# Kernel tuning notes

Measured on AMD Instinct MI355X. Metric: run time of the kernel, lower is better.

## Reference

```python
import jax, jax.numpy as jnp
import numpy as np

B, L, D, H = 2, 2048, 2048, 16
DH = D // H  # 128 per-head dim
EPS = 1e-5


def setup_inputs() -> dict:
    key = jax.random.key(0)
    ks = jax.random.split(key, 6)
    s = 0.02  # xavier-ish init scale with gain 2**-2.5
    return {
        "hidden_states": jax.random.normal(ks[0], (B, L, D), jnp.float32),
        "Wq": jax.random.normal(ks[1], (D, D), jnp.float32) * s,
        "Wk": jax.random.normal(ks[2], (D, D), jnp.float32) * s,
        "Wv": jax.random.normal(ks[3], (D, D), jnp.float32) * s,
        "Wb": jax.random.normal(ks[4], (D, H), jnp.float32) * s,
        "o_norm_weight": jnp.ones((DH,), jnp.float32),
        "Wo": jax.random.normal(ks[5], (D, D), jnp.float32) * s,
    }


def _delta_rule(q, k, v, beta):
    """Recurrent delta-rule linear attention.
    q,k,v: [B,H,L,Dh]; beta: [B,H,L]. Math identical to fused_chunk_delta_rule.
    S_t = S_{t-1} + k_t (beta_t * (v_t - S_{t-1}^T k_t))^T ;  o_t = S_t^T q_t
    """
    def step(S, inp):
        qt, kt, vt, bt = inp  # [B,H,Dh],[B,H,Dh],[B,H,Dh],[B,H]
        v_pred = jnp.einsum('bhk,bhkv->bhv', kt, S)
        delta = (vt - v_pred) * bt[..., None]
        S = S + kt[..., None] * delta[:, :, None, :]
        ot = jnp.einsum('bhk,bhkv->bhv', qt, S)
        return S, ot

    xs = (q.transpose(2, 0, 1, 3), k.transpose(2, 0, 1, 3),
          v.transpose(2, 0, 1, 3), beta.transpose(2, 0, 1))
    S0 = jnp.zeros(q.shape[:2] + (q.shape[-1], v.shape[-1]), q.dtype)
    _, o = jax.lax.scan(step, S0, xs)  # o: [L,B,H,Dh]
    return o.transpose(1, 2, 0, 3)  # [B,H,L,Dh]


def reference(hidden_states, Wq, Wk, Wv, Wb, o_norm_weight, Wo):
    b, l, d = hidden_states.shape
    h = Wb.shape[1]
    dh = d // h

    q = hidden_states @ Wq
    k = hidden_states @ Wk
    v = jax.nn.silu(hidden_states @ Wv)

    def heads(x):
        return x.reshape(b, l, h, dh).transpose(0, 2, 1, 3)  # b h l d

    q, k, v = heads(q), heads(k), heads(v)

    # qk_norm = 'l2' (torch F.normalize with eps clamp)
    def l2n(x):
        n = jnp.sqrt(jnp.sum(x * x, axis=-1, keepdims=True))
        return x / jnp.maximum(n, 1e-12)

    q, k = l2n(q), l2n(k)
    q = q * (dh ** -0.5)  # fla delta-rule default scale

    beta = jax.nn.sigmoid(hidden_states @ Wb).transpose(0, 2, 1)  # b h l

    o = _delta_rule(q, k, v, beta)  # b h l dh
    o = o.transpose(0, 2, 1, 3)  # b l h dh

    # RMSNorm over head_v_dim
    o = o * jax.lax.rsqrt(jnp.mean(o * o, axis=-1, keepdims=True) + EPS)
    o = o * o_norm_weight

    return o.reshape(b, l, d) @ Wo
```

## Files before the change

kernel.cpp:

```cpp
#include <hip/hip_runtime.h>
#include <hip/hip_bf16.h>
#include <cstdint>

#define DEV static __device__ __forceinline__

typedef unsigned short u16;
typedef unsigned int u32;
typedef __attribute__((ext_vector_type(8))) short short8;
typedef __attribute__((ext_vector_type(4))) float f32x4;

constexpr int Bn = 2, Ln = 2048, Dn = 2048, Hn = 16;
constexpr int Mrows = Bn * Ln;
constexpr int CHK = 64, NCK = Ln / CHK;
constexpr int NCHUNKS = Bn * Hn * NCK;

DEV float b2f(u16 s) { union { float f; u32 u; } x; x.u = ((u32)s) << 16; return x.f; }
DEV u16 f2b(float f) {
  union { float f; u32 u; } x; x.f = f; u32 u = x.u;
  return (u16)((u + 0x7fffu + ((u >> 16) & 1u)) >> 16);
}

DEV void cp16(const void* g, void* l) {
  __builtin_amdgcn_global_load_lds(
      (const __attribute__((address_space(1))) u32*)(unsigned long long)(g),
      (__attribute__((address_space(3))) u32*)(unsigned long long)(l), 16, 0, 0);
}

DEV f32x4 mfma16(short8 a, short8 b, f32x4 c) {
  return __builtin_amdgcn_mfma_f32_16x16x32_bf16(a, b, c, 0, 0, 0);
}

DEV short8 scale8(short8 v, float sc) {
  short8 o;
#pragma unroll
  for (int e = 0; e < 8; e++) o[e] = (short)f2b(b2f((u16)v[e]) * sc);
  return o;
}

__global__ void k_cvt(const float* __restrict__ src, u16* __restrict__ dst, int n8) {
  int i = blockIdx.x * blockDim.x + threadIdx.x;
  if (i >= n8) return;
  const float4* s4 = (const float4*)(src + (size_t)i * 8);
  float4 a = s4[0], b = s4[1];
  u16 o[8] = {f2b(a.x), f2b(a.y), f2b(a.z), f2b(a.w), f2b(b.x), f2b(b.y), f2b(b.z), f2b(b.w)};
  *(short8*)(dst + (size_t)i * 8) = *(short8*)o;
}

struct Trans2Args { const float* src[4]; u16* dst[4]; };
__global__ __launch_bounds__(256) void k_trans2(Trans2Args t) {
  __shared__ u16 tile[64][72];
  const float* src = t.src[blockIdx.z];
  u16* dst = t.dst[blockIdx.z];
  int r0 = blockIdx.y * 64, c0 = blockIdx.x * 64;
  int tid = threadIdx.x;
  int lr = tid >> 2, lc = (tid & 3) * 16;
  const float* s = src + (size_t)(r0 + lr) * 2048 + c0 + lc;
#pragma unroll
  for (int i = 0; i < 4; i++) {
    float4 v = *(const float4*)(s + i * 4);
    tile[lr][lc + i * 4 + 0] = f2b(v.x);
    tile[lr][lc + i * 4 + 1] = f2b(v.y);
    tile[lr][lc + i * 4 + 2] = f2b(v.z);
    tile[lr][lc + i * 4 + 3] = f2b(v.w);
  }
  __syncthreads();
  int orr = tid >> 2, oc = (tid & 3) * 16;
  u16* d = dst + (size_t)(c0 + orr) * 2048 + r0 + oc;
  u16 buf[16];
#pragma unroll
  for (int e = 0; e < 16; e++) buf[e] = tile[oc + e][orr];
  *(short8*)(d) = *(short8*)buf;
  *(short8*)(d + 8) = *(short8*)(buf + 8);
}

struct TransArgs {
  const float* src[1]; u16* dst[1]; int rows[1]; int cols[1];
};
__global__ void k_trans(TransArgs t) {
  __shared__ u16 tile[32][33];
  const float* src = t.src[0]; u16* dst = t.dst[0];
  int rows = t.rows[0], cols = t.cols[0];
  int r0 = blockIdx.y * 32, c0 = blockIdx.x * 32;
  if (r0 >= rows || c0 >= cols) return;
  int tx = threadIdx.x, ty = threadIdx.y;
  for (int i = ty; i < 32; i += 8) {
    int r = r0 + i, c = c0 + tx;
    if (r < rows && c < cols) tile[i][tx] = f2b(src[(size_t)r * cols + c]);
  }
  __syncthreads();
  for (int i = ty; i < 32; i += 8) {
    int r = c0 + i, c = r0 + tx;
    if (r < cols && c < rows) dst[(size_t)r * rows + c] = tile[tx][i];
  }
}

__global__ __launch_bounds__(256) void k_beta(const u16* __restrict__ hs,
                                              const u16* __restrict__ WbT,
                                              float* __restrict__ beta_g) {
  __shared__ float part[256];
  int tid = threadIdx.x, wave = tid >> 6, lane = tid & 63, quad = lane >> 4, l15 = lane & 15;
  int tok0 = blockIdx.x * 16;
  const u16* arow = hs + (size_t)(tok0 + l15) * Dn + wave * 512;
  const u16* brow = WbT + (size_t)l15 * Dn + wave * 512;
  f32x4 acc = {0.f, 0.f, 0.f, 0.f};
#pragma unroll
  for (int k = 0; k < 512; k += 32) {
    short8 af = *(const short8*)&arow[k + quad * 8];
    short8 bf = *(const short8*)&brow[k + quad * 8];
    acc = mfma16(af, bf, acc);
  }
  part[tid] = 0.f;
  __syncthreads();
#pragma unroll
  for (int r = 0; r < 4; r++) atomicAdd(&part[l15 * 16 + quad * 4 + r], acc[r]);
  __syncthreads();
  int h = tid >> 4, tr = tid & 15;
  int b = tok0 >> 11;
  int l = (tok0 + tr) & 2047;
  beta_g[(size_t)(b * Hn + h) * Ln + l] = 1.f / (1.f + __expf(-part[h * 16 + tr]));
}

struct Gemm2Args { const u16* A; const u16* Bt; u16* C; int K; };

__global__ __launch_bounds__(512, 2) void k_gemm2(Gemm2Args g) {
  __shared__ u16 ldsbuf[61440];
  const char* LB = (const char*)ldsbuf;
  const int K = g.K, NT = K / 64;
  const size_t Kb = (size_t)K * 2;
  int tid = threadIdx.x, wave = tid >> 6, lane = tid & 63;
  int quad = lane >> 4, l15 = lane & 15;
  int wm = wave >> 2, wn = wave & 3;

  int bid = blockIdx.x;
  int wg = (bid & 7) * 32 + (bid >> 3);
  int by = wg >> 4, bx = wg & 15;
  int m0 = by * 256, n0f = bx * 384;

  int r0 = tid >> 2;
  int cby = (((tid & 3) ^ ((tid >> 3) & 3)) * 16);
  const char* gA = (const char*)g.A + (size_t)(m0 + r0) * Kb + cby;
  const char* gB = (const char*)g.Bt + (size_t)(n0f + r0) * Kb + cby;

  auto stageA = [&](int slot, int t, int kh) {
    const char* src = gA + (size_t)t * 128 + kh * 64;
    u16* dst = &ldsbuf[slot * 8192 + tid * 8];
    cp16(src, dst);
    cp16(src + (size_t)128 * Kb, dst + 4096);
  };
  auto stageB = [&](int slot, int t, int kh) {
    const char* src = gB + (size_t)t * 128 + kh * 64;
    u16* dst = &ldsbuf[24576 + slot * 12288 + tid * 8];
    cp16(src, dst);
    cp16(src + (size_t)128 * Kb, dst + 4096);
    cp16(src + (size_t)256 * Kb, dst + 8192);
  };

  f32x4 acc0[4][6], acc1[4][6];
#pragma unroll
  for (int i = 0; i < 4; i++)
#pragma unroll
    for (int j = 0; j < 6; j++) {
      acc0[i][j] = (f32x4){0.f, 0.f, 0.f, 0.f};
      acc1[i][j] = (f32x4){0.f, 0.f, 0.f, 0.f};
    }

  int rsw = (l15 >> 1) & 3;
  int rA = (wm * 128 + l15) * 64 + ((quad ^ rsw) * 16);
  int rB = (wn * 96 + l15) * 64 + ((quad ^ rsw) * 16);

  stageA(0, 0, 0);
  stageB(0, 0, 0);
  stageA(1, 0, 1);
  stageB(1, 0, 1);

  short8 bf[6];
  int u0 = 0;
  for (int t = 0; t < NT; ++t) {
    int u1 = u0 + 1; if (u1 == 3) u1 = 0;
    int u2 = u1 + 1; if (u2 == 3) u2 = 0;
    bool pf = (t + 1 < NT);
    const char* aK0 = LB + u0 * 16384;
    const char* aK1 = LB + u1 * 16384;
    const char* bK0 = LB + 49152 + u0 * 24576;
    const char* bK1 = LB + 49152 + u1 * 24576;

    asm volatile("s_waitcnt vmcnt(5)" ::: "memory");
    __builtin_amdgcn_s_barrier();
    __builtin_amdgcn_sched_barrier(0);
    if (pf) stageA(u2, t + 1, 0);
    {
      short8 av[4];
#pragma unroll
      for (int i = 0; i < 4; i++) av[i] = *(const short8*)(aK0 + rA + i * 1024);
#pragma unroll
      for (int j = 0; j < 6; j++) bf[j] = *(const short8*)(bK0 + rB + j * 1024);
      __builtin_amdgcn_s_setprio(1);
#pragma unroll
      for (int i = 0; i < 4; i++)
#pragma unroll
        for (int j = 0; j < 6; j++) acc0[i][j] = mfma16(av[i], bf[j], acc0[i][j]);
      __builtin_amdgcn_s_setprio(0);
    }

    asm volatile("s_waitcnt vmcnt(5)" ::: "memory");
    __builtin_amdgcn_s_barrier();
    __builtin_amdgcn_sched_barrier(0);
    if (pf) stageB(u2, t + 1, 0);
    {
      short8 av[4];
#pragma unroll
      for (int i = 0; i < 4; i++) av[i] = *(const short8*)(aK0 + rA + 4096 + i * 1024);
      __builtin_amdgcn_s_setprio(1);
#pragma unroll
      for (int i = 0; i < 4; i++)
#pragma unroll
        for (int j = 0; j < 6; j++) acc1[i][j] = mfma16(av[i], bf[j], acc1[i][j]);
      __builtin_amdgcn_s_setprio(0);
    }

    if (t == NT - 1) asm volatile("s_waitcnt vmcnt(0)" ::: "memory");
    else asm volatile("s_waitcnt vmcnt(5)" ::: "memory");
    __builtin_amdgcn_s_barrier();
    __builtin_amdgcn_sched_barrier(0);
    if (pf) stageA(u0, t + 1, 1);
    {
      short8 av[4];
#pragma unroll
      for (int i = 0; i < 4; i++) av[i] = *(const short8*)(aK1 + rA + i * 1024);
#pragma unroll
      for (int j = 0; j < 6; j++) bf[j] = *(const short8*)(bK1 + rB + j * 1024);
      __builtin_amdgcn_s_setprio(1);
#pragma unroll
      for (int i = 0; i < 4; i++)
#pragma unroll
        for (int j = 0; j < 6; j++) acc0[i][j] = mfma16(av[i], bf[j], acc0[i][j]);
      __builtin_amdgcn_s_setprio(0);
    }

    asm volatile("s_waitcnt vmcnt(5)" ::: "memory");
    __builtin_amdgcn_s_barrier();
    __builtin_amdgcn_sched_barrier(0);
    if (pf) stageB(u0, t + 1, 1);
    {
      short8 av[4];
#pragma unroll
      for (int i = 0; i < 4; i++) av[i] = *(const short8*)(aK1 + rA + 4096 + i * 1024);
      __builtin_amdgcn_s_setprio(1);
#pragma unroll
      for (int i = 0; i < 4; i++)
#pragma unroll
        for (int j = 0; j < 6; j++) acc1[i][j] = mfma16(av[i], bf[j], acc1[i][j]);
      __builtin_amdgcn_s_setprio(0);
    }

    u0 = u2;
  }

#pragma unroll
  for (int mq = 0; mq < 2; mq++) {
#pragma unroll
    for (int i = 0; i < 4; i++)
#pragma unroll
      for (int j = 0; j < 6; j++) {
        f32x4 a = mq ? acc1[i][j] : acc0[i][j];
        int row = m0 + wm * 128 + mq * 64 + i * 16 + quad * 4;
        int colg = n0f + wn * 96 + j * 16;
        int z = colg >> 11;
        u16* Cz = g.C + (size_t)z * ((size_t)Mrows * 2048);
        int col = (colg & 2047) + l15;
#pragma unroll
        for (int r = 0; r < 4; r++) {
          float v = a[r];
          if (z == 2) v = v / (1.f + __expf(-v));
          Cz[(size_t)(row + r) * 2048 + col] = f2b(v);
        }
      }
  }
}

struct GemmoArgs { const u16* A; const u16* Bt; float* C; int K; };

__global__ __launch_bounds__(512, 2) void k_gemmo(GemmoArgs g) {
  __shared__ u16 ldsbuf[36864];
  const char* LB = (const char*)ldsbuf;
  const int K = g.K, NT = K / 64;
  const size_t Kb = (size_t)K * 2;
  int tid = threadIdx.x, wave = tid >> 6, lane = tid & 63;
  int quad = lane >> 4, l15 = lane & 15;
  int wm = wave >> 2, wn = wave & 3;

  int bid = blockIdx.x;
  int wg = (bid & 7) * 32 + (bid >> 3);
  int bx = wg >> 5, by = wg & 31;
  int m0 = by * 128, n0 = bx * 256;

  int r0 = tid >> 2;
  int cby = (((tid & 3) ^ ((tid >> 3) & 3)) * 16);
  const char* gA = (const char*)g.A + (size_t)(m0 + r0) * Kb + cby;
  const char* gB = (const char*)g.Bt + (size_t)(n0 + r0) * Kb + cby;

  auto stageA = [&](int slot, int t, int kh) {
    const char* src = gA + (size_t)t * 128 + kh * 64;
    cp16(src, &ldsbuf[slot * 4096 + tid * 8]);
  };
  auto stageB = [&](int slot, int t, int kh) {
    const char* src = gB + (size_t)t * 128 + kh * 64;
    u16* dst = &ldsbuf[12288 + slot * 8192 + tid * 8];
    cp16(src, dst);
    cp16(src + (size_t)128 * Kb, dst + 4096);
  };

  f32x4 acc[4][4];
#pragma unroll
  for (int i = 0; i < 4; i++)
#pragma unroll
    for (int j = 0; j < 4; j++) acc[i][j] = (f32x4){0.f, 0.f, 0.f, 0.f};

  int rsw = (l15 >> 1) & 3;
  int rA = (wm * 64 + l15) * 64 + ((quad ^ rsw) * 16);
  int rB = (wn * 64 + l15) * 64 + ((quad ^ rsw) * 16);

  stageA(0, 0, 0);
  stageB(0, 0, 0);
  stageA(1, 0, 1);
  stageB(1, 0, 1);

  short8 av[4];
  int u0 = 0;
  for (int t = 0; t < NT; ++t) {
    int u1 = u0 + 1; if (u1 == 3) u1 = 0;
    int u2 = u1 + 1; if (u2 == 3) u2 = 0;
    bool pf = (t + 1 < NT);
    const char* aK0 = LB + u0 * 8192;
    const char* aK1 = LB + u1 * 8192;
    const char* bK0 = LB + 24576 + u0 * 16384;
    const char* bK1 = LB + 24576 + u1 * 16384;

    asm volatile("s_waitcnt vmcnt(3)" ::: "memory");
    __builtin_amdgcn_s_barrier();
    __builtin_amdgcn_sched_barrier(0);
    if (pf) stageA(u2, t + 1, 0);
    {
      short8 bv[2];
#pragma unroll
      for (int i = 0; i < 4; i++) av[i] = *(const short8*)(aK0 + rA + i * 1024);
#pragma unroll
      for (int j = 0; j < 2; j++) bv[j] = *(const short8*)(bK0 + rB + j * 1024);
      __builtin_amdgcn_s_setprio(1);
#pragma unroll
      for (int i = 0; i < 4; i++)
#pragma unroll
        for (int j = 0; j < 2; j++) acc[i][j] = mfma16(av[i], bv[j], acc[i][j]);
      __builtin_amdgcn_s_setprio(0);
    }

    asm volatile("s_waitcnt vmcnt(3)" ::: "memory");
    __builtin_amdgcn_s_barrier();
    __builtin_amdgcn_sched_barrier(0);
    if (pf) stageB(u2, t + 1, 0);
    {
      short8 bv[2];
#pragma unroll
      for (int j = 0; j < 2; j++) bv[j] = *(const short8*)(bK0 + rB + (2 + j) * 1024);
      __builtin_amdgcn_s_setprio(1);
#pragma unroll
      for (int i = 0; i < 4; i++)
#pragma unroll
        for (int j = 0; j < 2; j++) acc[i][2 + j] = mfma16(av[i], bv[j], acc[i][2 + j]);
      __builtin_amdgcn_s_setprio(0);
    }

    if (t == NT - 1) asm volatile("s_waitcnt vmcnt(0)" ::: "memory");
    else asm volatile("s_waitcnt vmcnt(3)" ::: "memory");
    __builtin_amdgcn_s_barrier();
    __builtin_amdgcn_sched_barrier(0);
    if (pf) stageA(u0, t + 1, 1);
    {
      short8 bv[2];
#pragma unroll
      for (int i = 0; i < 4; i++) av[i] = *(const short8*)(aK1 + rA + i * 1024);
#pragma unroll
      for (int j = 0; j < 2; j++) bv[j] = *(const short8*)(bK1 + rB + j * 1024);
      __builtin_amdgcn_s_setprio(1);
#pragma unroll
      for (int i = 0; i < 4; i++)
#pragma unroll
        for (int j = 0; j < 2; j++) acc[i][j] = mfma16(av[i], bv[j], acc[i][j]);
      __builtin_amdgcn_s_setprio(0);
    }

    asm volatile("s_waitcnt vmcnt(3)" ::: "memory");
    __builtin_amdgcn_s_barrier();
    __builtin_amdgcn_sched_barrier(0);
    if (pf) stageB(u0, t + 1, 1);
    {
      short8 bv[2];
#pragma unroll
      for (int j = 0; j < 2; j++) bv[j] = *(const short8*)(bK1 + rB + (2 + j) * 1024);
      __builtin_amdgcn_s_setprio(1);
#pragma unroll
      for (int i = 0; i < 4; i++)
#pragma unroll
        for (int j = 0; j < 2; j++) acc[i][2 + j] = mfma16(av[i], bv[j], acc[i][2 + j]);
      __builtin_amdgcn_s_setprio(0);
    }

    u0 = u2;
  }

#pragma unroll
  for (int i = 0; i < 4; i++)
#pragma unroll
    for (int j = 0; j < 4; j++) {
      int row = m0 + wm * 64 + i * 16 + quad * 4;
      int col = n0 + wn * 64 + j * 16 + l15;
#pragma unroll
      for (int r = 0; r < 4; r++)
        g.C[(size_t)(row + r) * 2048 + col] = acc[i][j][r];
    }
}

constexpr int ST = 72;
__global__ __launch_bounds__(256, 4) void k_pre(
    const float* __restrict__ beta_g,
    const u16* __restrict__ qn, const u16* __restrict__ kn, const u16* __restrict__ vn,
    u16* __restrict__ W2g, u16* __restrict__ Ug, u16* __restrict__ Gg, u16* __restrict__ KTg,
    u16* __restrict__ Qg) {
  __shared__ float beta_s[64];
  __shared__ float rnk_s[64], rnq_s[64];
  __shared__ u16 mats[4 * 64 * ST];
  int gid = blockIdx.x;
  int c = gid & 31, h = (gid >> 5) & 15, b = gid >> 9;
  int tid = threadIdx.x;
  int l0 = c * 64;

  int wave = tid >> 6, lane = tid & 63, quad = lane >> 4, l15 = lane & 15;
  u16 *Br = mats, *Bc = mats + 64 * ST, *M0 = mats + 2 * 64 * ST, *M1 = mats + 3 * 64 * ST;

  short8 bfr[4], qfr[4];
  {
    int row = wave * 16 + l15;
    const u16* krow = kn + (size_t)(b * Ln + l0 + row) * Dn + h * 128;
    const u16* qrow = qn + (size_t)(b * Ln + l0 + row) * Dn + h * 128;
    float ssk = 0.f, ssq = 0.f;
#pragma unroll
    for (int s = 0; s < 4; s++) {
      bfr[s] = *(const short8*)&krow[quad * 8 + 32 * s];
      qfr[s] = *(const short8*)&qrow[quad * 8 + 32 * s];
#pragma unroll
      for (int e = 0; e < 8; e++) {
        float xk = b2f((u16)bfr[s][e]), xq = b2f((u16)qfr[s][e]);
        ssk += xk * xk; ssq += xq * xq;
      }
    }
    ssk += __shfl_xor(ssk, 16, 64); ssk += __shfl_xor(ssk, 32, 64);
    ssq += __shfl_xor(ssq, 16, 64); ssq += __shfl_xor(ssq, 32, 64);
    float rk = 1.f / fmaxf(sqrtf(ssk), 1e-12f);
    float rq = 0.08838834764831845f / fmaxf(sqrtf(ssq), 1e-12f);
    if (quad == 0) { rnk_s[row] = rk; rnq_s[row] = rq; }
#pragma unroll
    for (int s = 0; s < 4; s++) {
      bfr[s] = scale8(bfr[s], rk);
      *(short8*)&Qg[(size_t)gid * 8192 + (size_t)row * 128 + quad * 8 + 32 * s] =
          scale8(qfr[s], rq);
    }
  }
  if (tid < 64) beta_s[tid] = beta_g[(size_t)(b * Hn + h) * Ln + l0 + tid];
  __syncthreads();

  {
#pragma unroll
    for (int mt = 0; mt < 4; ++mt) {
      const u16* arow_k = kn + (size_t)(b * Ln + l0 + mt * 16 + l15) * Dn + h * 128;
      const u16* arow_q = qn + (size_t)(b * Ln + l0 + mt * 16 + l15) * Dn + h * 128;
      float rkA = rnk_s[mt * 16 + l15], rqA = rnq_s[mt * 16 + l15];
      f32x4 accA = {0.f, 0.f, 0.f, 0.f}, accG = {0.f, 0.f, 0.f, 0.f};
#pragma unroll
      for (int s = 0; s < 4; s++) {
        short8 ak = scale8(*(const short8*)&arow_k[quad * 8 + 32 * s], rkA);
        short8 aq = scale8(*(const short8*)&arow_q[quad * 8 + 32 * s], rqA);
        accA = mfma16(ak, bfr[s], accA);
        accG = mfma16(aq, bfr[s], accG);
      }
      int t = wave * 16 + l15;
#pragma unroll
      for (int r = 0; r < 4; r++) {
        int i = mt * 16 + quad * 4 + r;
        u16 nb = f2b((t < i) ? -beta_s[i] * accA[r] : 0.f);
        Br[i * ST + t] = nb;
        Bc[t * ST + i] = nb;
        M0[i * ST + t] = (t == i) ? f2b(1.f) : nb;
        Gg[(size_t)gid * 4096 + (size_t)i * 64 + t] = f2b((t <= i) ? accG[r] : 0.f);
      }
    }
  }
  __syncthreads();

  u16 *Mc = M0, *Mn = M1;
#pragma unroll
  for (int it = 0; it < 5; ++it) {
    const int tT = (it < 3) ? 0 : ((it == 3) ? 1 : 2);
    const int tI = (it < 4) ? 0 : 1;
    short8 bb[2];
#pragma unroll
    for (int s = 0; s < 2; s++) bb[s] = *(const short8*)&Bc[(wave * 16 + l15) * ST + quad * 8 + 32 * s];
    f32x4 accT[4];
#pragma unroll
    for (int mt = 0; mt < 4; mt++) {
      accT[mt] = (f32x4){0.f, 0.f, 0.f, 0.f};
      if (mt - wave >= tT) {
#pragma unroll
        for (int s = 0; s < 2; s++) {
          short8 af = *(const short8*)&Br[(mt * 16 + l15) * ST + quad * 8 + 32 * s];
          accT[mt] = mfma16(af, bb[s], accT[mt]);
        }
      }
    }
    __syncthreads();
#pragma unroll
    for (int mt = 0; mt < 4; mt++) {
      if (mt - wave >= tI) {
#pragma unroll
        for (int r = 0; r < 4; r++) {
          int i = mt * 16 + quad * 4 + r, t = wave * 16 + l15;
          u16 v = f2b(accT[mt][r]);
          Br[i * ST + t] = v;
          Bc[t * ST + i] = v;
        }
      }
    }
    __syncthreads();
    short8 tb[2];
#pragma unroll
    for (int s = 0; s < 2; s++) tb[s] = *(const short8*)&Bc[(wave * 16 + l15) * ST + quad * 8 + 32 * s];
#pragma unroll
    for (int mt = 0; mt < 4; mt++) {
      if (mt - wave >= tT) {
        f32x4 a;
#pragma unroll
        for (int r = 0; r < 4; r++) a[r] = b2f(Mc[(mt * 16 + quad * 4 + r) * ST + wave * 16 + l15]);
#pragma unroll
        for (int s = 0; s < 2; s++) {
          short8 af = *(const short8*)&Mc[(mt * 16 + l15) * ST + quad * 8 + 32 * s];
          a = mfma16(af, tb[s], a);
        }
#pragma unroll
        for (int r = 0; r < 4; r++) Mn[(mt * 16 + quad * 4 + r) * ST + wave * 16 + l15] = f2b(a[r]);
      } else {
#pragma unroll
        for (int r = 0; r < 4; r++)
          Mn[(mt * 16 + quad * 4 + r) * ST + wave * 16 + l15] =
              Mc[(mt * 16 + quad * 4 + r) * ST + wave * 16 + l15];
      }
    }
    u16* tmp = Mc; Mc = Mn; Mn = tmp;
  }
  __syncthreads();

  u16* XT = mats;
  u16* Mb = Mn;
  for (int idx = tid; idx < 512; idx += 256) {
    int i = idx >> 3, t8 = (idx & 7) * 8;
    short8 m8 = *(const short8*)&Mc[i * ST + t8];
    short8 o8;
#pragma unroll
    for (int e = 0; e < 8; e++) o8[e] = (short)f2b(b2f((u16)m8[e]) * beta_s[t8 + e]);
    *(short8*)&Mb[i * ST + t8] = o8;
  }
  int tv = tid & 63, dk0 = (tid >> 6) * 32;
  for (int pass = 0; pass < 2; ++pass) {
    const u16* src = pass ? vn : kn;
    const u16* srow = src + (size_t)(b * Ln + l0 + tv) * Dn + h * 128 + dk0;
    float rsc = pass ? 1.f : rnk_s[tv];
#pragma unroll
    for (int s = 0; s < 4; s++) {
      short8 vv = *(const short8*)&srow[s * 8];
      if (!pass) vv = scale8(vv, rsc);
#pragma unroll
      for (int e = 0; e < 8; e++) XT[(dk0 + s * 8 + e) * ST + tv] = (u16)vv[e];
    }
    __syncthreads();
    if (pass == 0) {
#pragma unroll
      for (int it2 = 0; it2 < 4; it2++) {
        int idx = tid + it2 * 256;
        int dk = idx >> 3, t0 = (idx & 7) * 8;
        *(short8*)&KTg[(size_t)gid * 8192 + dk * 64 + t0] =
            *(const short8*)&XT[dk * ST + t0];
      }
    }
    u16* dst = pass ? Ug : W2g;
#pragma unroll
    for (int half = 0; half < 2; ++half) {
      int nt = wave + half * 4;
      short8 bx[2];
#pragma unroll
      for (int s = 0; s < 2; s++) bx[s] = *(const short8*)&XT[(nt * 16 + l15) * ST + quad * 8 + 32 * s];
#pragma unroll
      for (int mt = 0; mt < 4; mt++) {
        f32x4 a = {0.f, 0.f, 0.f, 0.f};
#pragma unroll
        for (int s = 0; s < 2; s++) {
          short8 af = *(const short8*)&Mb[(mt * 16 + l15) * ST + quad * 8 + 32 * s];
          a = mfma16(af, bx[s], a);
        }
#pragma unroll
        for (int r = 0; r < 4; r++)
          dst[(size_t)gid * 8192 + (size_t)(mt * 16 + quad * 4 + r) * 128 + nt * 16 + l15] = f2b(a[r]);
      }
    }
    __syncthreads();
  }
}

struct Frg { short8 w2[4], qf[4], gf[2], k0[2], k1[2]; float u[4]; };

__global__ __launch_bounds__(256) void k_scan(
    const u16* __restrict__ Qg, const u16* __restrict__ W2g, const u16* __restrict__ Ug,
    const u16* __restrict__ Gg, const u16* __restrict__ KTg, u16* __restrict__ Og) {
  constexpr int SST = 136, DST = 104;
  __shared__ u16 Sb[16 * SST];
  __shared__ u16 Db[16 * DST];
  int bh = blockIdx.x, sl = blockIdx.y;
  int b = bh >> 4, h = bh & 15, c0 = sl * 16;
  int tid = threadIdx.x, wave = tid >> 6, lane = tid & 63, quad = lane >> 4, l15 = lane & 15;
  for (int i = tid; i < 16 * SST; i += 256) Sb[i] = 0;
  f32x4 accS0 = {0.f, 0.f, 0.f, 0.f}, accS1 = {0.f, 0.f, 0.f, 0.f};
  __syncthreads();

  auto load_frags = [&](Frg& F, int ci) {
    size_t ck = (size_t)bh * NCK + ci;
    const u16* w2row = W2g + ck * 8192 + (size_t)(wave * 16 + l15) * 128;
    const u16* qrow = Qg + ck * 8192 + (size_t)(wave * 16 + l15) * 128;
#pragma unroll
    for (int s = 0; s < 4; s++) {
      F.w2[s] = *(const short8*)&w2row[quad * 8 + 32 * s];
      F.qf[s] = *(const short8*)&qrow[quad * 8 + 32 * s];
    }
    const u16* grow = Gg + ck * 4096 + (size_t)(wave * 16 + l15) * 64;
    const u16* kt0 = KTg + ck * 8192 + (size_t)(wave * 16 + l15) * 64;
    const u16* kt1 = KTg + ck * 8192 + (size_t)((wave + 4) * 16 + l15) * 64;
#pragma unroll
    for (int s = 0; s < 2; s++) {
      F.gf[s] = *(const short8*)&grow[quad * 8 + 32 * s];
      F.k0[s] = *(const short8*)&kt0[quad * 8 + 32 * s];
      F.k1[s] = *(const short8*)&kt1[quad * 8 + 32 * s];
    }
    const u16* urow = Ug + ck * 8192 + (size_t)(wave * 16 + quad * 4) * 128 + c0 + l15;
#pragma unroll
    for (int r = 0; r < 4; r++) F.u[r] = b2f(urow[(size_t)r * 128]);
  };

  auto compute = [&](const Frg& F, int ci) {
    f32x4 accT = {0.f, 0.f, 0.f, 0.f}, accO = {0.f, 0.f, 0.f, 0.f};
#pragma unroll
    for (int s = 0; s < 4; s++) {
      short8 sf = *(const short8*)&Sb[l15 * SST + quad * 8 + 32 * s];
      accT = mfma16(F.w2[s], sf, accT);
      accO = mfma16(F.qf[s], sf, accO);
    }
#pragma unroll
    for (int r = 0; r < 4; r++) {
      float d = F.u[r] - accT[r];
      Db[l15 * DST + wave * 16 + quad * 4 + r] = f2b(d);
    }
    __syncthreads();
#pragma unroll
    for (int s = 0; s < 2; s++) {
      short8 df = *(const short8*)&Db[l15 * DST + quad * 8 + 32 * s];
      accO = mfma16(F.gf[s], df, accO);
      accS0 = mfma16(F.k0[s], df, accS0);
      accS1 = mfma16(F.k1[s], df, accS1);
    }
    u16* orow = Og + (size_t)(b * Ln + ci * 64 + wave * 16 + quad * 4) * Dn + h * 128 + c0 + l15;
#pragma unroll
    for (int r = 0; r < 4; r++) orow[(size_t)r * Dn] = f2b(accO[r]);
#pragma unroll
    for (int r = 0; r < 4; r++) {
      Sb[l15 * SST + wave * 16 + quad * 4 + r] = f2b(accS0[r]);
      Sb[l15 * SST + (wave + 4) * 16 + quad * 4 + r] = f2b(accS1[r]);
    }
    __syncthreads();
  };

  Frg FA, FB;
  load_frags(FA, 0);
  for (int ci = 0; ci < NCK; ci += 2) {
    load_frags(FB, ci + 1);
    compute(FA, ci);
    if (ci + 2 < NCK) load_frags(FA, ci + 2);
    compute(FB, ci + 1);
  }
}

__global__ void k_rms(const u16* __restrict__ Og, const float* __restrict__ w, u16* __restrict__ out) {
  int tid = threadIdx.x, wave = tid >> 6, lane = tid & 63;
  size_t row = (size_t)blockIdx.x * 4 + wave;
  const u16* p = Og + row * 128;
  u32 u = *(const u32*)&p[lane * 2];
  float x0 = b2f((u16)(u & 0xffff)), x1 = b2f((u16)(u >> 16));
  float ss = x0 * x0 + x1 * x1;
#pragma unroll
  for (int o = 32; o > 0; o >>= 1) ss += __shfl_xor(ss, o, 64);
  float sc = rsqrtf(ss * (1.f / 128.f) + 1e-5f);
  float w0 = w[lane * 2], w1 = w[lane * 2 + 1];
  u32 o2 = (u32)f2b(x0 * sc * w0) | ((u32)f2b(x1 * sc * w1) << 16);
  *(u32*)&out[row * 128 + lane * 2] = o2;
}

extern "C" void kernel_launch(void* const* d_in, const int* in_sizes, int n_in,
                              void* d_out, int out_size, void* d_ws, size_t ws_size,
                              hipStream_t stream) {
  (void)in_sizes; (void)n_in; (void)out_size; (void)ws_size;
  const float* hs_f = (const float*)d_in[0];
  const float* Wq = (const float*)d_in[1];
  const float* Wk = (const float*)d_in[2];
  const float* Wv = (const float*)d_in[3];
  const float* Wb = (const float*)d_in[4];
  const float* onw = (const float*)d_in[5];
  const float* Wo = (const float*)d_in[6];

  char* ws = (char*)d_ws;
  size_t off = 0;
  auto alloc = [&](size_t bytes) -> void* {
    void* p = ws + off;
    off += (bytes + 255) & ~(size_t)255;
    return p;
  };
  const size_t WB = (size_t)2048 * 2048 * 2;
  const size_t XB = (size_t)4096 * 2048 * 2;
  u16* WqT = (u16*)alloc(WB);
  u16* WkT = (u16*)alloc(WB);
  u16* WvT = (u16*)alloc(WB);
  u16* WoT = (u16*)alloc(WB);
  u16* WbT = (u16*)alloc((size_t)16 * 2048 * 2);
  u16* hsb = (u16*)alloc(XB);
  u16* qn  = (u16*)alloc(XB);
  u16* kn  = (u16*)alloc(XB);
  u16* vn  = (u16*)alloc(XB);
  u16* W2g = (u16*)alloc((size_t)NCHUNKS * 8192 * 2);
  u16* Ug  = (u16*)alloc((size_t)NCHUNKS * 8192 * 2);
  u16* Gg  = (u16*)alloc((size_t)NCHUNKS * 4096 * 2);
  u16* KTg = (u16*)alloc((size_t)NCHUNKS * 8192 * 2);
  u16* Qg  = (u16*)alloc((size_t)NCHUNKS * 8192 * 2);
  float* beta_g = (float*)alloc((size_t)Bn * Hn * Ln * 4);
  u16* Og = vn;
  u16* onorm = qn;

  hipLaunchKernelGGL(k_cvt, dim3(Mrows * Dn / 8 / 256), dim3(256), 0, stream, hs_f, hsb, Mrows * Dn / 8);

  Trans2Args t2;
  t2.src[0] = Wq; t2.dst[0] = WqT;
  t2.src[1] = Wk; t2.dst[1] = WkT;
  t2.src[2] = Wv; t2.dst[2] = WvT;
  t2.src[3] = Wo; t2.dst[3] = WoT;
  hipLaunchKernelGGL(k_trans2, dim3(32, 32, 4), dim3(256), 0, stream, t2);
  TransArgs ta;
  ta.src[0] = Wb; ta.dst[0] = WbT; ta.rows[0] = 2048; ta.cols[0] = 16;
  hipLaunchKernelGGL(k_trans, dim3(1, 64, 1), dim3(32, 8), 0, stream, ta);

  hipLaunchKernelGGL(k_beta, dim3(Mrows / 16), dim3(256), 0, stream, hsb, WbT, beta_g);

  {
    Gemm2Args g2;
    g2.A = hsb; g2.Bt = WqT; g2.C = qn; g2.K = 2048;
    hipLaunchKernelGGL(k_gemm2, dim3(256), dim3(512), 0, stream, g2);
  }

  hipLaunchKernelGGL(k_pre, dim3(NCHUNKS), dim3(256), 0, stream,
                     beta_g, qn, kn, vn, W2g, Ug, Gg, KTg, Qg);

  hipLaunchKernelGGL(k_scan, dim3(32, 8), dim3(256), 0, stream,
                     Qg, W2g, Ug, Gg, KTg, Og);

  hipLaunchKernelGGL(k_rms, dim3(16384), dim3(256), 0, stream, Og, onw, onorm);

  {
    GemmoArgs go;
    go.A = onorm; go.Bt = WoT; go.C = (float*)d_out; go.K = 2048;
    hipLaunchKernelGGL(k_gemmo, dim3(256), dim3(512), 0, stream, go);
  }
}
```

Baseline: 418.1 us.

## Rewrite fused QKV GEMM with 256x256 tiles and quadrant-staged double buffering

Replaces the fused QKV projection GEMM (256x384 tiles, triple-buffered K-halves, 256 blocks) with a 256x256-tile kernel over 384 blocks. Each K=64 step now runs as four quadrant phases that reuse A and B fragments across sub-tiles, with prefetch of A one step ahead and B two steps ahead into 128 KB of LDS. The LDS layout uses a new XOR swizzle. Launch bounds drop to one block per CU, trading occupancy for larger per-block reuse and a finer overlap of loads with MFMA work, and 384 blocks may not fill the CUs in even waves.

```diff
diff --git a/kernel.cpp b/kernel.cpp
--- a/kernel.cpp
+++ b/kernel.cpp
@@ -120,162 +120,159 @@
   beta_g[(size_t)(b * Hn + h) * Ln + l] = 1.f / (1.f + __expf(-part[h * 16 + tr]));
 }
 
-struct Gemm2Args { const u16* A; const u16* Bt; u16* C; int K; };
-
-__global__ __launch_bounds__(512, 2) void k_gemm2(Gemm2Args g) {
-  __shared__ u16 ldsbuf[61440];
-  const char* LB = (const char*)ldsbuf;
-  const int K = g.K, NT = K / 64;
-  const size_t Kb = (size_t)K * 2;
+struct Gemm3Args { const u16* A; const u16* Bt; u16* C; int K; };
+
+__global__ __launch_bounds__(512, 1) void k_gemm3(Gemm3Args g) {
+  __shared__ u16 sh3[65536];
+  const int NT = g.K / 64;
+  const size_t Kb = (size_t)g.K * 2;
   int tid = threadIdx.x, wave = tid >> 6, lane = tid & 63;
   int quad = lane >> 4, l15 = lane & 15;
   int wm = wave >> 2, wn = wave & 3;
 
   int bid = blockIdx.x;
-  int wg = (bid & 7) * 32 + (bid >> 3);
-  int by = wg >> 4, bx = wg & 15;
-  int m0 = by * 256, n0f = bx * 384;
-
-  int r0 = tid >> 2;
-  int cby = (((tid & 3) ^ ((tid >> 3) & 3)) * 16);
-  const char* gA = (const char*)g.A + (size_t)(m0 + r0) * Kb + cby;
-  const char* gB = (const char*)g.Bt + (size_t)(n0f + r0) * Kb + cby;
-
-  auto stageA = [&](int slot, int t, int kh) {
-    const char* src = gA + (size_t)t * 128 + kh * 64;
-    u16* dst = &ldsbuf[slot * 8192 + tid * 8];
-    cp16(src, dst);
-    cp16(src + (size_t)128 * Kb, dst + 4096);
+  int wg = (bid & 7) * 48 + (bid >> 3);
+  int by = wg / 24, bx = wg - by * 24;
+  int m0 = by * 256, n0 = bx * 256;
+
+  int scb = ((lane & 7) ^ (lane >> 3)) * 16;
+  const char* gA = (const char*)g.A + (size_t)(m0 + wave * 16 + (lane >> 3)) * Kb + scb;
+  const char* gB = (const char*)g.Bt + (size_t)(n0 + wave * 16 + (lane >> 3)) * Kb + scb;
+  u16* dst0 = &sh3[wave * 1024 + lane * 8];
+
+  auto stA = [&](int d, int h, int t) {
+    const char* src = gA + (size_t)(h * 128) * Kb + (size_t)t * 128;
+    u16* dp = dst0 + (d * 2 + h) * 8192;
+    cp16(src, dp);
+    cp16(src + (size_t)8 * Kb, dp + 512);
   };
-  auto stageB = [&](int slot, int t, int kh) {
-    const char* src = gB + (size_t)t * 128 + kh * 64;
-    u16* dst = &ldsbuf[24576 + slot * 12288 + tid * 8];
-    cp16(src, dst);
-    cp16(src + (size_t)128 * Kb, dst + 4096);
-    cp16(src + (size_t)256 * Kb, dst + 8192);
+  auto stB = [&](int d, int h, int t) {
+    const char* src = gB + (size_t)(h * 128) * Kb + (size_t)t * 128;
+    u16* dp = dst0 + 32768 + (d * 2 + h) * 8192;
+    cp16(src, dp);
+    cp16(src + (size_t)8 * Kb, dp + 512);
   };
 
-  f32x4 acc0[4][6], acc1[4][6];
-#pragma unroll
-  for (int i = 0; i < 4; i++)
-#pragma unroll
-    for (int j = 0; j < 6; j++) {
-      acc0[i][j] = (f32x4){0.f, 0.f, 0.f, 0.f};
-      acc1[i][j] = (f32x4){0.f, 0.f, 0.f, 0.f};
-    }
-
-  int rsw = (l15 >> 1) & 3;
-  int rA = (wm * 128 + l15) * 64 + ((quad ^ rsw) * 16);
-  int rB = (wn * 96 + l15) * 64 + ((quad ^ rsw) * 16);
-
-  stageA(0, 0, 0);
-  stageB(0, 0, 0);
-  stageA(1, 0, 1);
-  stageB(1, 0, 1);
-
-  short8 bf[6];
-  int u0 = 0;
-  for (int t = 0; t < NT; ++t) {
-    int u1 = u0 + 1; if (u1 == 3) u1 = 0;
-    int u2 = u1 + 1; if (u2 == 3) u2 = 0;
-    bool pf = (t + 1 < NT);
-    const char* aK0 = LB + u0 * 16384;
-    const char* aK1 = LB + u1 * 16384;
-    const char* bK0 = LB + 49152 + u0 * 24576;
-    const char* bK1 = LB + 49152 + u1 * 24576;
-
-    asm volatile("s_waitcnt vmcnt(5)" ::: "memory");
-    __builtin_amdgcn_s_barrier();
+  f32x4 acc[8][4];
+#pragma unroll
+  for (int i = 0; i < 8; i++)
+#pragma unroll
+    for (int j = 0; j < 4; j++) acc[i][j] = (f32x4){0.f, 0.f, 0.f, 0.f};
+  short8 av[4][2], b0[2][2], b1[2][2];
+
+  int cbk0 = (quad ^ (l15 & 7)) * 16;
+  int aro = l15 * 128;
+  int bro = ((wn & 1) * 64 + l15) * 128;
+
+  stB(0, 0, 0); stB(0, 1, 0);
+  stA(0, 0, 0); stA(0, 1, 0);
+  stB(1, 0, 1); stB(1, 1, 1);
+  asm volatile("s_waitcnt vmcnt(4)" ::: "memory");
+  __builtin_amdgcn_s_barrier();
+
+  for (int T = 0; T < NT; ++T) {
+    int d = T & 1, dn = d ^ 1;
+    const char* aBs = (const char*)sh3 + (d * 2 + wm) * 16384;
+    const char* bBs = (const char*)sh3 + 65536 + (d * 2 + (wn >> 1)) * 16384;
+    bool pfA = (T + 1 < NT), pfB = (T + 2 < NT);
+
+#pragma unroll
+    for (int ii = 0; ii < 4; ii++) {
+      av[ii][0] = *(const short8*)(aBs + aro + ii * 2048 + cbk0);
+      av[ii][1] = *(const short8*)(aBs + aro + ii * 2048 + (cbk0 ^ 64));
+    }
+#pragma unroll
+    for (int jj = 0; jj < 2; jj++) {
+      b0[jj][0] = *(const short8*)(bBs + bro + jj * 2048 + cbk0);
+      b0[jj][1] = *(const short8*)(bBs + bro + jj * 2048 + (cbk0 ^ 64));
+    }
+    if (pfA) stA(dn, 0, T + 1);
+    __builtin_amdgcn_s_barrier();
+    asm volatile("s_waitcnt lgkmcnt(0)" ::: "memory");
     __builtin_amdgcn_sched_barrier(0);
-    if (pf) stageA(u2, t + 1, 0);
-    {
-      short8 av[4];
-#pragma unroll
-      for (int i = 0; i < 4; i++) av[i] = *(const short8*)(aK0 + rA + i * 1024);
-#pragma unroll
-      for (int j = 0; j < 6; j++) bf[j] = *(const short8*)(bK0 + rB + j * 1024);
-      __builtin_amdgcn_s_setprio(1);
-#pragma unroll
-      for (int i = 0; i < 4; i++)
-#pragma unroll
-        for (int j = 0; j < 6; j++) acc0[i][j] = mfma16(av[i], bf[j], acc0[i][j]);
-      __builtin_amdgcn_s_setprio(0);
-    }
-
-    asm volatile("s_waitcnt vmcnt(5)" ::: "memory");
-    __builtin_amdgcn_s_barrier();
+    __builtin_amdgcn_s_setprio(1);
+#pragma unroll
+    for (int ii = 0; ii < 4; ii++)
+#pragma unroll
+      for (int jj = 0; jj < 2; jj++) {
+        acc[ii][jj] = mfma16(av[ii][0], b0[jj][0], acc[ii][jj]);
+        acc[ii][jj] = mfma16(av[ii][1], b0[jj][1], acc[ii][jj]);
+      }
+    __builtin_amdgcn_s_setprio(0);
+    __builtin_amdgcn_s_barrier();
+
+#pragma unroll
+    for (int jj = 0; jj < 2; jj++) {
+      b1[jj][0] = *(const short8*)(bBs + bro + 4096 + jj * 2048 + cbk0);
+      b1[jj][1] = *(const short8*)(bBs + bro + 4096 + jj * 2048 + (cbk0 ^ 64));
+    }
+    if (pfA) stA(dn, 1, T + 1);
+    __builtin_amdgcn_s_barrier();
+    asm volatile("s_waitcnt lgkmcnt(0)" ::: "memory");
     __builtin_amdgcn_sched_barrier(0);
-    if (pf) stageB(u2, t + 1, 0);
-    {
-      short8 av[4];
-#pragma unroll
-      for (int i = 0; i < 4; i++) av[i] = *(const short8*)(aK0 + rA + 4096 + i * 1024);
-      __builtin_amdgcn_s_setprio(1);
-#pragma unroll
-      for (int i = 0; i < 4; i++)
-#pragma unroll
-        for (int j = 0; j < 6; j++) acc1[i][j] = mfma16(av[i], bf[j], acc1[i][j]);
-      __builtin_amdgcn_s_setprio(0);
-    }
-
-    if (t == NT - 1) asm volatile("s_waitcnt vmcnt(0)" ::: "memory");
-    else asm volatile("s_waitcnt vmcnt(5)" ::: "memory");
-    __builtin_amdgcn_s_barrier();
+    __builtin_amdgcn_s_setprio(1);
+#pragma unroll
+    for (int ii = 0; ii < 4; ii++)
+#pragma unroll
+      for (int jj = 0; jj < 2; jj++) {
+        acc[ii][2 + jj] = mfma16(av[ii][0], b1[jj][0], acc[ii][2 + jj]);
+        acc[ii][2 + jj] = mfma16(av[ii][1], b1[jj][1], acc[ii][2 + jj]);
+      }
+    __builtin_amdgcn_s_setprio(0);
+    __builtin_amdgcn_s_barrier();
+
+#pragma unroll
+    for (int ii = 0; ii < 4; ii++) {
+      av[ii][0] = *(const short8*)(aBs + 8192 + aro + ii * 2048 + cbk0);
+      av[ii][1] = *(const short8*)(aBs + 8192 + aro + ii * 2048 + (cbk0 ^ 64));
+    }
+    if (pfB) stB(d, 0, T + 2);
+    __builtin_amdgcn_s_barrier();
+    asm volatile("s_waitcnt lgkmcnt(0)" ::: "memory");
     __builtin_amdgcn_sched_barrier(0);
-    if (pf) stageA(u0, t + 1, 1);
-    {
-      short8 av[4];
-#pragma unroll
-      for (int i = 0; i < 4; i++) av[i] = *(const short8*)(aK1 + rA + i * 1024);
-#pragma unroll
-      for (int j = 0; j < 6; j++) bf[j] = *(const short8*)(bK1 + rB + j * 1024);
-      __builtin_amdgcn_s_setprio(1);
-#pragma unroll
-      for (int i = 0; i < 4; i++)
-#pragma unroll
-        for (int j = 0; j < 6; j++) acc0[i][j] = mfma16(av[i], bf[j], acc0[i][j]);
-      __builtin_amdgcn_s_setprio(0);
-    }
-
-    asm volatile("s_waitcnt vmcnt(5)" ::: "memory");
-    __builtin_amdgcn_s_barrier();
-    __builtin_amdgcn_sched_barrier(0);
-    if (pf) stageB(u0, t + 1, 1);
-    {
-      short8 av[4];
-#pragma unroll
-      for (int i = 0; i < 4; i++) av[i] = *(const short8*)(aK1 + rA + 4096 + i * 1024);
-      __builtin_amdgcn_s_setprio(1);
-#pragma unroll
-      for (int i = 0; i < 4; i++)
-#pragma unroll
-        for (int j = 0; j < 6; j++) acc1[i][j] = mfma16(av[i], bf[j], acc1[i][j]);
-      __builtin_amdgcn_s_setprio(0);
-    }
-
-    u0 = u2;
-  }
-
-#pragma unroll
-  for (int mq = 0; mq < 2; mq++) {
-#pragma unroll
-    for (int i = 0; i < 4; i++)
-#pragma unroll
-      for (int j = 0; j < 6; j++) {
-        f32x4 a = mq ? acc1[i][j] : acc0[i][j];
-        int row = m0 + wm * 128 + mq * 64 + i * 16 + quad * 4;
-        int colg = n0f + wn * 96 + j * 16;
-        int z = colg >> 11;
-        u16* Cz = g.C + (size_t)z * ((size_t)Mrows * 2048);
-        int col = (colg & 2047) + l15;
-#pragma unroll
-        for (int r = 0; r < 4; r++) {
-          float v = a[r];
-          if (z == 2) v = v / (1.f + __expf(-v));
-          Cz[(size_t)(row + r) * 2048 + col] = f2b(v);
-        }
-      }
-  }
+    __builtin_amdgcn_s_setprio(1);
+#pragma unroll
+    for (int ii = 0; ii < 4; ii++)
+#pragma unroll
+      for (int jj = 0; jj < 2; jj++) {
+        acc[4 + ii][2 + jj] = mfma16(av[ii][0], b1[jj][0], acc[4 + ii][2 + jj]);
+        acc[4 + ii][2 + jj] = mfma16(av[ii][1], b1[jj][1], acc[4 + ii][2 + jj]);
+      }
+    __builtin_amdgcn_s_setprio(0);
+    __builtin_amdgcn_s_barrier();
+
+    if (pfB) stB(d, 1, T + 2);
+    __builtin_amdgcn_s_setprio(1);
+#pragma unroll
+    for (int ii = 0; ii < 4; ii++)
+#pragma unroll
+      for (int jj = 0; jj < 2; jj++) {
+        acc[4 + ii][jj] = mfma16(av[ii][0], b0[jj][0], acc[4 + ii][jj]);
+        acc[4 + ii][jj] = mfma16(av[ii][1], b0[jj][1], acc[4 + ii][jj]);
+      }
+    __builtin_amdgcn_s_setprio(0);
+    if (T == NT - 2) asm volatile("s_waitcnt vmcnt(0)" ::: "memory");
+    else if (T < NT - 2) asm volatile("s_waitcnt vmcnt(4)" ::: "memory");
+    __builtin_amdgcn_s_barrier();
+  }
+
+  int z = n0 >> 11;
+  u16* Cz = g.C + (size_t)z * ((size_t)Mrows * 2048);
+  int colb = (n0 & 2047) + wn * 64;
+  int rowb = m0 + wm * 128;
+#pragma unroll
+  for (int i = 0; i < 8; i++)
+#pragma unroll
+    for (int j = 0; j < 4; j++) {
+      int row = rowb + i * 16 + quad * 4;
+      int col = colb + j * 16 + l15;
+#pragma unroll
+      for (int r = 0; r < 4; r++) {
+        float v = acc[i][j][r];
+        if (z == 2) v = v / (1.f + __expf(-v));
+        Cz[(size_t)(row + r) * 2048 + col] = f2b(v);
+      }
+    }
 }
 
 struct GemmoArgs { const u16* A; const u16* Bt; float* C; int K; };
@@ -762,9 +759,9 @@
   hipLaunchKernelGGL(k_beta, dim3(Mrows / 16), dim3(256), 0, stream, hsb, WbT, beta_g);
 
   {
-    Gemm2Args g2;
-    g2.A = hsb; g2.Bt = WqT; g2.C = qn; g2.K = 2048;
-    hipLaunchKernelGGL(k_gemm2, dim3(256), dim3(512), 0, stream, g2);
+    Gemm3Args g3;
+    g3.A = hsb; g3.Bt = WqT; g3.C = qn; g3.K = 2048;
+    hipLaunchKernelGGL(k_gemm3, dim3(384), dim3(512), 0, stream, g3);
   }
 
   hipLaunchKernelGGL(k_pre, dim3(NCHUNKS), dim3(256), 0, stream,
```

Measured after the change: 439.7 us. +5.1%, slower.
